# Optimization experiments

Hardware: AMD Instinct MI355X
Metric: run time of the kernel (lower is better)

The kernel has to match this reference:

```python
import jax, jax.numpy as jnp
import numpy as np

E = 768      # embed_size
H = 12       # num_heads inside each nn.MultiheadAttention
G = 4        # num_groups
D = E // H   # per-head dim = 64


def setup_inputs() -> dict:
    key = jax.random.key(0)
    ks = jax.random.split(key, 20)
    s = 0.02
    B, S = 2, 2048
    inp = {
        "query": jax.random.normal(ks[0], (B, S, E), jnp.float32),
        "key":   jax.random.normal(ks[1], (B, S, E), jnp.float32),
        "value": jax.random.normal(ks[2], (B, S, E), jnp.float32),
        # outer projections (query_group_proj / key_proj / value_proj)
        "Wqg": jax.random.normal(ks[3], (E, E), jnp.float32) * s,
        "bqg": jnp.zeros((E,), jnp.float32),
        "Wk":  jax.random.normal(ks[4], (E, E), jnp.float32) * s,
        "bk":  jnp.zeros((E,), jnp.float32),
        "Wv":  jax.random.normal(ks[5], (E, E), jnp.float32) * s,
        "bv":  jnp.zeros((E,), jnp.float32),
        # per-group MultiheadAttention params (in_proj split into q/k/v, out_proj)
        "Wq_in": jax.random.normal(ks[6], (G, E, E), jnp.float32) * s,
        "bq_in": jnp.zeros((G, E), jnp.float32),
        "Wk_in": jax.random.normal(ks[7], (G, E, E), jnp.float32) * s,
        "bk_in": jnp.zeros((G, E), jnp.float32),
        "Wv_in": jax.random.normal(ks[8], (G, E, E), jnp.float32) * s,
        "bv_in": jnp.zeros((G, E), jnp.float32),
        "Wout":  jax.random.normal(ks[9], (G, E, E), jnp.float32) * s,
        "bout":  jnp.zeros((G, E), jnp.float32),
    }
    return inp


def reference(query, key, value, Wqg, bqg, Wk, bk, Wv, bv,
              Wq_in, bq_in, Wk_in, bk_in, Wv_in, bv_in, Wout, bout):
    B, S, _ = query.shape
    T = S // G  # tokens per group
    scale = 1.0 / np.sqrt(D).astype(np.float32)

    # outer projections (Linear: x @ W.T + b)
    q = query @ Wqg.T + bqg                         # [B,S,E]
    k = key   @ Wk.T  + bk                          # [B,S,E]
    v = value @ Wv.T  + bv                          # [B,S,E]

    # split query tokens into G interleaved groups (view + permute in source)
    qg = q.reshape(B, T, G, E).transpose(0, 2, 1, 3)  # [B,G,T,E]

    # per-group MHA input projections (batched over groups)
    qi = jnp.einsum('bgte,gfe->bgtf', qg, Wq_in) + bq_in[None, :, None, :]
    ki = jnp.einsum('bse,gfe->bgsf', k,  Wk_in) + bk_in[None, :, None, :]
    vi = jnp.einsum('bse,gfe->bgsf', v,  Wv_in) + bv_in[None, :, None, :]

    qh = qi.reshape(B, G, T, H, D)
    kh = ki.reshape(B, G, S, H, D)
    vh = vi.reshape(B, G, S, H, D)

    scores = jnp.einsum('bgthd,bgshd->bghts', qh, kh) * scale  # [B,G,H,T,S]
    attn = jax.nn.softmax(scores, axis=-1)
    ctx = jnp.einsum('bghts,bgshd->bgthd', attn, vh).reshape(B, G, T, E)

    out_g = jnp.einsum('bgte,gfe->bgtf', ctx, Wout) + bout[None, :, None, :]  # [B,G,T,E]

    # reassemble sequence order (inverse of the grouping permutation)
    out = out_g.transpose(0, 2, 1, 3).reshape(B, S, E)
    return out
```

## Files before the change

kernel.cpp:

```cpp
#include <hip/hip_runtime.h>
#include <hip/hip_bf16.h>


typedef __attribute__((ext_vector_type(8))) short short8;
typedef __attribute__((ext_vector_type(4))) float floatx4;

static __device__ __forceinline__ short f2bf(float f) {
    __bf16 b = (__bf16)f;
    return __builtin_bit_cast(short, b);
}
static __device__ __forceinline__ short8 f8_to_bf8(floatx4 f0, floatx4 f1) {
    short8 s;
    s[0]=f2bf(f0[0]); s[1]=f2bf(f0[1]); s[2]=f2bf(f0[2]); s[3]=f2bf(f0[3]);
    s[4]=f2bf(f1[0]); s[5]=f2bf(f1[1]); s[6]=f2bf(f1[2]); s[7]=f2bf(f1[3]);
    return s;
}
static __device__ __forceinline__ void gload_lds16(const short* g, short* l) {
    __builtin_amdgcn_global_load_lds(
        (const __attribute__((address_space(1))) unsigned int*)g,
        (__attribute__((address_space(3))) unsigned int*)l, 16, 0, 0);
}

__global__ __launch_bounds__(256) void cast_w(
    const float* a0, const float* a1, const float* a2, const float* a3,
    const float* a4, const float* a5, const float* a6, short* dst)
{
    const long U = 589824L;
    const float* ptrs[7] = {a0,a1,a2,a3,a4,a5,a6};
    const long starts[8] = {0, U, 2*U, 3*U, 7*U, 11*U, 15*U, 19*U};
    long i = (long)blockIdx.x * 2048 + (long)threadIdx.x * 8;
    int t = 0;
    while (t < 6 && i >= starts[t + 1]) t++;
    const float* s = ptrs[t] + (i - starts[t]);
    floatx4 f0 = *(const floatx4*)s;
    floatx4 f1 = *(const floatx4*)(s + 4);
    *(short8*)(dst + i) = f8_to_bf8(f0, f1);
}

#define GEMM_LANE_VARS                                                        \
    const int tid = threadIdx.x, lane = tid & 63, w = tid >> 6;               \
    const int wm = w & 1, wn = w >> 1;                                        \
    const int qr = lane >> 4, lc = lane & 15, x7 = lc & 7;                    \
    const int srow = tid >> 3, schunk = tid & 7, sx = srow & 7;

template<int CMODE, int BIAS_MODE>
static __device__ __forceinline__ void gemm_epilogue(
    floatx4 (&acc)[4][4], const float* bp, void* Cv, int ldc, int bm, int bn,
    int wm, int wn, int qr, int lc)
{
#pragma unroll
    for (int ni = 0; ni < 4; ni++) {
        const int gcol = bn * 128 + wn * 64 + ni * 16 + lc;
        const float bcol = (BIAS_MODE == 0) ? bp[gcol] : 0.f;
#pragma unroll
        for (int mi = 0; mi < 4; mi++) {
#pragma unroll
            for (int r = 0; r < 4; r++) {
                const int grow = bm * 128 + wm * 64 + mi * 16 + qr * 4 + r;
                const float bb = (BIAS_MODE == 1) ? bp[grow] : bcol;
                const float v = acc[mi][ni][r] + bb;
                if (CMODE == 0)
                    ((short*)Cv)[(long)grow * ldc + gcol] = f2bf(v);
                else
                    ((float*)Cv)[(long)grow * ldc + gcol] = v;
            }
        }
    }
}

static __device__ __forceinline__ void gemm_mfma_step(
    floatx4 (&acc)[4][4], const short* Ac, const short* Bc,
    int wm, int wn, int qr, int lc, int x7)
{
#pragma unroll
    for (int ks = 0; ks < 64; ks += 32) {
        const int c0 = (ks >> 3) + qr;
        const int slot = ((c0 ^ x7) << 3);
        short8 af[4], bfr[4];
#pragma unroll
        for (int mi = 0; mi < 4; mi++)
            af[mi] = *(const short8*)&Ac[(wm * 64 + mi * 16 + lc) * 64 + slot];
#pragma unroll
        for (int ni = 0; ni < 4; ni++)
            bfr[ni] = *(const short8*)&Bc[(wn * 64 + ni * 16 + lc) * 64 + slot];
#pragma unroll
        for (int mi = 0; mi < 4; mi++)
#pragma unroll
            for (int ni = 0; ni < 4; ni++)
                acc[mi][ni] = __builtin_amdgcn_mfma_f32_16x16x32_bf16(
                    af[mi], bfr[ni], acc[mi][ni], 0, 0, 0);
    }
}

template<int CMODE, int BIAS_MODE>
static __device__ __forceinline__ void gemm_core_db(
    const short* __restrict__ A, const short* __restrict__ Wb,
    const float* __restrict__ bp, void* __restrict__ Cv,
    int lda, int ldc, int bm, int bn, short* As, short* Bs)
{
    GEMM_LANE_VARS
    const short* Ab = A + (long)(bm * 128) * lda;
    const short* Wt = Wb + (long)(bn * 128) * 768;
    const int gch = ((schunk ^ sx) << 3);

    floatx4 acc[4][4];
#pragma unroll
    for (int mi = 0; mi < 4; mi++)
#pragma unroll
        for (int ni = 0; ni < 4; ni++) acc[mi][ni] = (floatx4){0.f, 0.f, 0.f, 0.f};

#pragma unroll
    for (int p = 0; p < 4; p++) {
        gload_lds16(Ab + (long)(p * 32 + srow) * lda + gch, &As[(p * 32 + w * 8) * 64]);
        gload_lds16(Wt + (long)(p * 32 + srow) * 768 + gch, &Bs[(p * 32 + w * 8) * 64]);
    }

    for (int kk = 0; kk < 12; kk++) {
        __syncthreads();
        if (kk < 11) {
            const int k1 = (kk + 1) * 64;
            const int nb = ((kk + 1) & 1) * 8192;
#pragma unroll
            for (int p = 0; p < 4; p++) {
                gload_lds16(Ab + (long)(p * 32 + srow) * lda + k1 + gch,
                            &As[nb + (p * 32 + w * 8) * 64]);
                gload_lds16(Wt + (long)(p * 32 + srow) * 768 + k1 + gch,
                            &Bs[nb + (p * 32 + w * 8) * 64]);
            }
        }
        gemm_mfma_step(acc, As + (kk & 1) * 8192, Bs + (kk & 1) * 8192,
                       wm, wn, qr, lc, x7);
    }
    gemm_epilogue<CMODE, BIAS_MODE>(acc, bp, Cv, ldc, bm, bn, wm, wn, qr, lc);
}

template<int CMODE, int BIAS_MODE>
static __device__ __forceinline__ void gemm_core_f32(
    const float* __restrict__ A, const short* __restrict__ Wb,
    const float* __restrict__ bp, void* __restrict__ Cv,
    int lda, int ldc, int bm, int bn, short* As, short* Bs)
{
    GEMM_LANE_VARS
    const short* Wt = Wb + (long)(bn * 128) * 768;

    floatx4 acc[4][4];
#pragma unroll
    for (int mi = 0; mi < 4; mi++)
#pragma unroll
        for (int ni = 0; ni < 4; ni++) acc[mi][ni] = (floatx4){0.f, 0.f, 0.f, 0.f};

    for (int k0 = 0; k0 < 768; k0 += 64) {
        __syncthreads();
#pragma unroll
        for (int p = 0; p < 4; p++) {
            const int row = p * 32 + srow;
            const float* ap = A + (long)(bm * 128 + row) * lda + k0 + schunk * 8;
            floatx4 f0 = *(const floatx4*)ap;
            floatx4 f1 = *(const floatx4*)(ap + 4);
            *(short8*)&As[row * 64 + ((schunk ^ sx) << 3)] = f8_to_bf8(f0, f1);
            gload_lds16(Wt + (long)row * 768 + k0 + ((schunk ^ sx) << 3),
                        &Bs[(p * 32 + w * 8) * 64]);
        }
        __syncthreads();
        gemm_mfma_step(acc, As, Bs, wm, wn, qr, lc, x7);
    }
    gemm_epilogue<CMODE, BIAS_MODE>(acc, bp, Cv, ldc, bm, bn, wm, wn, qr, lc);
}

__global__ __launch_bounds__(256) void qkv_gemm(
    const float* q, const float* k, const float* v, const short* Wbf,
    const float* bq, const float* bk, const float* bv, short* outp)
{
    __shared__ short As[128 * 64];
    __shared__ short Bs[128 * 64];
    const int xcd = blockIdx.x & 7, slot = blockIdx.x >> 3;
    const int bm = xcd * 4 + slot / 18;
    const int rem = slot % 18, y = rem / 6, bn = rem % 6;
    const float* A    = (y == 0) ? q  : (y == 1) ? k  : v;
    const float* bias = (y == 0) ? bq : (y == 1) ? bk : bv;
    gemm_core_f32<0, 0>(A, Wbf + (long)y * 589824, bias, outp + (long)y * 3145728,
                        768, 768, bm, bn, As, Bs);
}

__global__ __launch_bounds__(256) void mid_gemm(
    const short* kproj, const short* vproj, const short* qproj, const short* Wbf,
    const float* bq_in, const float* bk_in, const float* bv_in,
    short* kiB, short* vtB, short* qiB)
{
    extern __shared__ short sm[];
    short* As = sm;
    short* Bs = sm + 16384;
    const int xcd = blockIdx.x & 7, slot = blockIdx.x >> 3;
    const int z = xcd, b = z >> 2, g = z & 3;
    if (slot < 96) {
        gemm_core_db<0, 0>(kproj + (long)b * 1572864, Wbf + (long)(7 + g) * 589824,
                           bk_in + g * 768, kiB + (long)z * 1572864,
                           768, 768, slot / 6, slot % 6, As, Bs);
    } else if (slot < 192) {
        const int s2 = slot - 96;
        gemm_core_db<0, 1>(Wbf + (long)(11 + g) * 589824, vproj + (long)b * 1572864,
                           bv_in + g * 768, vtB + (long)z * 1572864,
                           768, 2048, s2 / 16, s2 % 16, As, Bs);
    } else {
        const int s3 = slot - 192;
        gemm_core_db<0, 0>(qproj + (long)b * 1572864 + g * 768, Wbf + (long)(3 + g) * 589824,
                           bq_in + g * 768, qiB + (long)z * 393216,
                           3072, 768, s3 / 6, s3 % 6, As, Bs);
    }
}

__global__ __launch_bounds__(256) void out_gemm(
    const short* ctxB, const short* Wbf, const float* bout, float* out)
{
    extern __shared__ short sm[];
    short* As = sm;
    short* Bs = sm + 16384;
    const int xcd = blockIdx.x & 7, slot = blockIdx.x >> 3;
    const int z = xcd, b = z >> 2, g = z & 3;
    gemm_core_db<2, 0>(ctxB + (long)z * 393216, Wbf + (long)(15 + g) * 589824,
                       bout + g * 768, out + (long)b * 1572864 + g * 768,
                       768, 3072, slot / 6, slot % 6, As, Bs);
}

__global__ __launch_bounds__(256) void attn_kernel(
    const short* __restrict__ qi, const short* __restrict__ ki,
    const short* __restrict__ vt, short* __restrict__ ctx)
{
    __shared__ short Kt[2][64 * 64];
    __shared__ short Vt[2][64 * 64];
    __shared__ short Ps[4][16 * 64];

    const int tid = threadIdx.x, lane = tid & 63, w = tid >> 6;
    const int qr = lane >> 4, lc = lane & 15, x7 = lc & 7;
    const int headid = blockIdx.x % 96;
    const int tile = blockIdx.x / 96;
    const int h = headid % 12, bg = headid / 12;

    const short* qp = qi + ((long)bg * 512 + tile * 64 + w * 16 + lc) * 768 + h * 64 + qr * 8;
    const short8 aq0 = *(const short8*)qp;
    const short8 aq1 = *(const short8*)(qp + 32);

    const short one = (lc == 0) ? (short)0x3F80 : (short)0;
    const short8 onesv = (short8){one, one, one, one, one, one, one, one};

    floatx4 cacc[4], lacc = (floatx4){0.f, 0.f, 0.f, 0.f};
#pragma unroll
    for (int dc = 0; dc < 4; dc++) cacc[dc] = (floatx4){0.f, 0.f, 0.f, 0.f};

    const int srow = lane >> 3, schk = lane & 7, swz = schk ^ srow;
    const short* kgb = ki + ((long)bg * 2048) * 768 + h * 64;
    const short* vgb = vt + ((long)(bg * 768 + h * 64)) * 2048;

#pragma unroll
    for (int inst = 0; inst < 2; inst++) {
        const int rk = w * 16 + inst * 8 + srow;
        gload_lds16(kgb + (long)rk * 768 + swz * 8, &Kt[0][(w * 16 + inst * 8) * 64]);
        gload_lds16(vgb + (long)rk * 2048 + swz * 8, &Vt[0][(w * 16 + inst * 8) * 64]);
    }

    for (int it = 0; it < 32; it++) {
        const int cur = it & 1;
        __syncthreads();
        if (it < 31) {
            const int nxt = cur ^ 1, s0 = (it + 1) * 64;
#pragma unroll
            for (int inst = 0; inst < 2; inst++) {
                const int rk = w * 16 + inst * 8 + srow;
                gload_lds16(kgb + (long)(s0 + rk) * 768 + swz * 8,
                            &Kt[nxt][(w * 16 + inst * 8) * 64]);
                gload_lds16(vgb + (long)rk * 2048 + s0 + swz * 8,
                            &Vt[nxt][(w * 16 + inst * 8) * 64]);
            }
        }

        const short* Kb = &Kt[cur][0];
        const short* Vb = &Vt[cur][0];

        floatx4 sv[4];
#pragma unroll
        for (int ss = 0; ss < 4; ss++) {
            const short* kr = Kb + (ss * 16 + lc) * 64;
            short8 b0 = *(const short8*)(kr + ((qr ^ x7) << 3));
            short8 b1 = *(const short8*)(kr + (((4 + qr) ^ x7) << 3));
            floatx4 t = (floatx4){0.f, 0.f, 0.f, 0.f};
            t = __builtin_amdgcn_mfma_f32_16x16x32_bf16(aq0, b0, t, 0, 0, 0);
            t = __builtin_amdgcn_mfma_f32_16x16x32_bf16(aq1, b1, t, 0, 0, 0);
            sv[ss] = t;
        }

        short* ps = &Ps[w][0];
#pragma unroll
        for (int ss = 0; ss < 4; ss++) {
            const int cch = ss * 2 + (lc >> 3);
#pragma unroll
            for (int r = 0; r < 4; r++) {
                const int m = qr * 4 + r;
                ps[m * 64 + ((cch ^ (m & 7)) << 3) + x7] =
                    f2bf(__builtin_amdgcn_exp2f(sv[ss][r] * 0.18033688f));
            }
        }
        asm volatile("s_waitcnt lgkmcnt(0)" ::: "memory");
        const short8 ap0 = *(const short8*)&ps[lc * 64 + ((qr ^ x7) << 3)];
        const short8 ap1 = *(const short8*)&ps[lc * 64 + (((4 + qr) ^ x7) << 3)];

        lacc = __builtin_amdgcn_mfma_f32_16x16x32_bf16(ap0, onesv, lacc, 0, 0, 0);
        lacc = __builtin_amdgcn_mfma_f32_16x16x32_bf16(ap1, onesv, lacc, 0, 0, 0);
#pragma unroll
        for (int dc = 0; dc < 4; dc++) {
            const short* vr = Vb + (dc * 16 + lc) * 64;
            short8 bv0 = *(const short8*)(vr + ((qr ^ x7) << 3));
            short8 bv1 = *(const short8*)(vr + (((4 + qr) ^ x7) << 3));
            cacc[dc] = __builtin_amdgcn_mfma_f32_16x16x32_bf16(ap0, bv0, cacc[dc], 0, 0, 0);
            cacc[dc] = __builtin_amdgcn_mfma_f32_16x16x32_bf16(ap1, bv1, cacc[dc], 0, 0, 0);
        }
    }

    float linv[4];
#pragma unroll
    for (int r = 0; r < 4; r++)
        linv[r] = 1.f / __shfl(lacc[r], lane & 48);
    short* cp = ctx + ((long)bg * 512 + tile * 64 + w * 16) * 768 + h * 64;
#pragma unroll
    for (int dc = 0; dc < 4; dc++)
#pragma unroll
        for (int r = 0; r < 4; r++)
            cp[(qr * 4 + r) * 768 + dc * 16 + lc] = f2bf(cacc[dc][r] * linv[r]);
}

extern "C" void kernel_launch(void* const* d_in, const int* in_sizes, int n_in,
                              void* d_out, int out_size, void* d_ws, size_t ws_size,
                              hipStream_t stream) {
    const float* query = (const float*)d_in[0];
    const float* key   = (const float*)d_in[1];
    const float* value = (const float*)d_in[2];
    const float* Wqg = (const float*)d_in[3];  const float* bqg = (const float*)d_in[4];
    const float* Wk  = (const float*)d_in[5];  const float* bk  = (const float*)d_in[6];
    const float* Wv  = (const float*)d_in[7];  const float* bv  = (const float*)d_in[8];
    const float* Wq_in = (const float*)d_in[9];  const float* bq_in = (const float*)d_in[10];
    const float* Wk_in = (const float*)d_in[11]; const float* bk_in = (const float*)d_in[12];
    const float* Wv_in = (const float*)d_in[13]; const float* bv_in = (const float*)d_in[14];
    const float* Wout  = (const float*)d_in[15]; const float* bout  = (const float*)d_in[16];
    float* out = (float*)d_out;

    short* ws     = (short*)d_ws;
    short* Wbf    = ws;
    short* q_proj = ws + 11206656L;
    short* k_proj = ws + 14352384L;
    short* v_proj = ws + 17498112L;
    short* qiB    = ws + 20643840L;
    short* vtB    = ws + 23789568L;
    short* kiB    = ws + 36372480L;
    short* ctxB   = ws + 11206656L;

    dim3 blk(256);

    cast_w<<<dim3(5472), blk, 0, stream>>>(
        Wqg, Wk, Wv, Wq_in, Wk_in, Wv_in, Wout, Wbf);

    qkv_gemm<<<dim3(576), blk, 0, stream>>>(
        query, key, value, Wbf, bqg, bk, bv, q_proj);

    mid_gemm<<<dim3(1728), blk, 65536, stream>>>(
        k_proj, v_proj, q_proj, Wbf, bq_in, bk_in, bv_in, kiB, vtB, qiB);

    attn_kernel<<<dim3(768), blk, 0, stream>>>(qiB, kiB, vtB, ctxB);

    out_gemm<<<dim3(192), blk, 65536, stream>>>(ctxB, Wbf, bout, out);
}
```

Baseline: 299.5 us.

## Replace mid GEMM with 256x256-tile 512-thread double-buffered MFMA kernel

Adds a new GEMM core that computes 256x256 output tiles with 8 waves, where each wave owns a 128x64 sub-tile. It double-buffers 64-wide K slices in LDS using direct global-to-LDS loads, an XOR-swizzled layout, and phased MFMA issue with priority boosting. The mid projection kernel now launches 432 large blocks instead of 1728 smaller ones, which raises operand reuse per LDS load and cuts global traffic. The trade-off is 128KB of LDS per block, so only one block fits per CU. With 432 blocks there is also a risk of load imbalance across CUs and higher register pressure.

Result: slower. 319.7 us (+6.7%).

```diff
diff --git a/kernel.cpp b/kernel.cpp
--- a/kernel.cpp
+++ b/kernel.cpp
@@ -182,30 +182,134 @@
                         768, 768, bm, bn, As, Bs);
 }
 
-__global__ __launch_bounds__(256) void mid_gemm(
+template<int BIAS_MODE>
+static __device__ __forceinline__ void gemm256_core(
+    const short* __restrict__ A, const short* __restrict__ B,
+    const float* __restrict__ bias, short* __restrict__ C,
+    int lda, int ldc, int bm, int bn, short* As, short* Bs)
+{
+    const int tid = threadIdx.x, lane = tid & 63, w = tid >> 6;
+    const int wm = w & 1, wn = w >> 1;
+    const int qr = lane >> 4, lc = lane & 15, x7 = lc & 7;
+    const int srow = tid >> 3, schunk = tid & 7;
+    const int gch = ((schunk ^ (srow & 7)) << 3);
+
+    const short* Ab = A + (long)(bm * 256) * lda;
+    const short* Bb = B + (long)(bn * 256) * 768;
+
+    floatx4 acc[8][4];
+#pragma unroll
+    for (int i = 0; i < 8; i++)
+#pragma unroll
+        for (int j = 0; j < 4; j++) acc[i][j] = (floatx4){0.f, 0.f, 0.f, 0.f};
+
+#pragma unroll
+    for (int r = 0; r < 256; r += 64) {
+        gload_lds16(Ab + (long)(r + srow) * lda + gch, As + (r + w * 8) * 64);
+        gload_lds16(Bb + (long)(r + srow) * 768 + gch, Bs + (r + w * 8) * 64);
+    }
+
+#pragma unroll 1
+    for (int kt = 0; kt < 12; ++kt) {
+        const int s = kt & 1;
+        if (kt < 11) {
+            short* Ad = As + (1 - s) * 16384;
+            short* Bd = Bs + (1 - s) * 16384;
+            const int koff = (kt + 1) * 64;
+#pragma unroll
+            for (int r = 0; r < 256; r += 64) {
+                gload_lds16(Ab + (long)(r + srow) * lda + koff + gch,
+                            Ad + (r + w * 8) * 64);
+                gload_lds16(Bb + (long)(r + srow) * 768 + koff + gch,
+                            Bd + (r + w * 8) * 64);
+            }
+            asm volatile("s_waitcnt vmcnt(8)" ::: "memory");
+        } else {
+            asm volatile("s_waitcnt vmcnt(0)" ::: "memory");
+        }
+        __builtin_amdgcn_s_barrier();
+
+        const short* Ac = As + s * 16384;
+        const short* Bc = Bs + s * 16384;
+        short8 af[4][2], bfr[2][2];
+#pragma unroll
+        for (int ph = 0; ph < 4; ++ph) {
+            const int mh = ph >> 1, nh = ph & 1;
+            if (nh == 0) {
+#pragma unroll
+                for (int mi = 0; mi < 4; mi++)
+#pragma unroll
+                    for (int ks = 0; ks < 2; ks++)
+                        af[mi][ks] = *(const short8*)&Ac[
+                            (wm * 128 + (mh * 4 + mi) * 16 + lc) * 64 +
+                            ((((ks << 2) + qr) ^ x7) << 3)];
+            }
+#pragma unroll
+            for (int ni = 0; ni < 2; ni++)
+#pragma unroll
+                for (int ks = 0; ks < 2; ks++)
+                    bfr[ni][ks] = *(const short8*)&Bc[
+                        (wn * 64 + (nh * 2 + ni) * 16 + lc) * 64 +
+                        ((((ks << 2) + qr) ^ x7) << 3)];
+            __builtin_amdgcn_s_barrier();
+            asm volatile("s_waitcnt lgkmcnt(0)" ::: "memory");
+            __builtin_amdgcn_sched_barrier(0);
+            __builtin_amdgcn_s_setprio(1);
+#pragma unroll
+            for (int ks = 0; ks < 2; ks++)
+#pragma unroll
+                for (int mi = 0; mi < 4; mi++)
+#pragma unroll
+                    for (int ni = 0; ni < 2; ni++)
+                        acc[mh * 4 + mi][nh * 2 + ni] =
+                            __builtin_amdgcn_mfma_f32_16x16x32_bf16(
+                                af[mi][ks], bfr[ni][ks],
+                                acc[mh * 4 + mi][nh * 2 + ni], 0, 0, 0);
+            __builtin_amdgcn_s_setprio(0);
+            __builtin_amdgcn_sched_barrier(0);
+            __builtin_amdgcn_s_barrier();
+        }
+    }
+
+#pragma unroll
+    for (int ni = 0; ni < 4; ni++) {
+        const int gcol = bn * 256 + wn * 64 + ni * 16 + lc;
+        const float bcol = (BIAS_MODE == 0) ? bias[gcol] : 0.f;
+#pragma unroll
+        for (int mi = 0; mi < 8; mi++) {
+#pragma unroll
+            for (int r = 0; r < 4; r++) {
+                const int grow = bm * 256 + wm * 128 + mi * 16 + qr * 4 + r;
+                const float bb = (BIAS_MODE == 1) ? bias[grow] : bcol;
+                C[(long)grow * ldc + gcol] = f2bf(acc[mi][ni][r] + bb);
+            }
+        }
+    }
+}
+
+__global__ __launch_bounds__(512, 2) void mid_gemm2(
     const short* kproj, const short* vproj, const short* qproj, const short* Wbf,
     const float* bq_in, const float* bk_in, const float* bv_in,
     short* kiB, short* vtB, short* qiB)
 {
-    extern __shared__ short sm[];
-    short* As = sm;
-    short* Bs = sm + 16384;
+    __shared__ short As[2 * 16384];
+    __shared__ short Bs[2 * 16384];
     const int xcd = blockIdx.x & 7, slot = blockIdx.x >> 3;
     const int z = xcd, b = z >> 2, g = z & 3;
-    if (slot < 96) {
-        gemm_core_db<0, 0>(kproj + (long)b * 1572864, Wbf + (long)(7 + g) * 589824,
-                           bk_in + g * 768, kiB + (long)z * 1572864,
-                           768, 768, slot / 6, slot % 6, As, Bs);
-    } else if (slot < 192) {
-        const int s2 = slot - 96;
-        gemm_core_db<0, 1>(Wbf + (long)(11 + g) * 589824, vproj + (long)b * 1572864,
-                           bv_in + g * 768, vtB + (long)z * 1572864,
-                           768, 2048, s2 / 16, s2 % 16, As, Bs);
+    if (slot < 24) {
+        gemm256_core<0>(kproj + (long)b * 1572864, Wbf + (long)(7 + g) * 589824,
+                        bk_in + g * 768, kiB + (long)z * 1572864,
+                        768, 768, slot / 3, slot % 3, As, Bs);
+    } else if (slot < 48) {
+        const int s2 = slot - 24;
+        gemm256_core<1>(Wbf + (long)(11 + g) * 589824, vproj + (long)b * 1572864,
+                        bv_in + g * 768, vtB + (long)z * 1572864,
+                        768, 2048, s2 / 8, s2 % 8, As, Bs);
     } else {
-        const int s3 = slot - 192;
-        gemm_core_db<0, 0>(qproj + (long)b * 1572864 + g * 768, Wbf + (long)(3 + g) * 589824,
-                           bq_in + g * 768, qiB + (long)z * 393216,
-                           3072, 768, s3 / 6, s3 % 6, As, Bs);
+        const int s3 = slot - 48;
+        gemm256_core<0>(qproj + (long)b * 1572864 + g * 768, Wbf + (long)(3 + g) * 589824,
+                        bq_in + g * 768, qiB + (long)z * 393216,
+                        3072, 768, s3 / 3, s3 % 3, As, Bs);
     }
 }
 
@@ -360,7 +464,7 @@
     qkv_gemm<<<dim3(576), blk, 0, stream>>>(
         query, key, value, Wbf, bqg, bk, bv, q_proj);
 
-    mid_gemm<<<dim3(1728), blk, 65536, stream>>>(
+    mid_gemm2<<<dim3(432), dim3(512), 0, stream>>>(
         k_proj, v_proj, q_proj, Wbf, bq_in, bk_in, bv_in, kiB, vtB, qiB);
 
     attn_kernel<<<dim3(768), blk, 0, stream>>>(qiB, kiB, vtB, ctxB);
```
